# Kernel optimization log

Hardware: AMD Instinct MI355X
Metric: run time of the kernel (lower is better)

## Reference

```python
import jax, jax.numpy as jnp
import numpy as np
from jax import lax

# 4D convolution via lax.conv_general_dilated (supports N spatial dims natively)
# Layout: x is (N, C, T, U, V, W); weight is (O, I, kT, kU, kV, kW)

def conv4d(x, w, b):
    dn = lax.conv_dimension_numbers(x.shape, w.shape, ('NCTUVW', 'OITUVW', 'NCTUVW'))
    y = lax.conv_general_dilated(x, w, window_strides=(1, 1, 1, 1), padding='SAME',
                                 dimension_numbers=dn)
    return y + b[None, :, None, None, None, None]


def setup_inputs() -> dict:
    key = jax.random.key(0)
    k0, k1, k2, k3, k4 = jax.random.split(key, 5)
    B, C_in, C_hid, C_out = 2, 64, 128, 64
    T, D, H, W = 4, 16, 32, 32
    K = 3  # kernel size per dim (stmode 'C' -> (3,3,3,3))
    x = jax.random.normal(k0, (B, C_in, T, D, H, W), dtype=jnp.float32)
    scale1 = 1.0 / np.sqrt(C_in * K ** 4)
    scale2 = 1.0 / np.sqrt(C_hid * K ** 4)
    w1 = jax.random.normal(k1, (C_hid, C_in, K, K, K, K), dtype=jnp.float32) * scale1
    b1 = jax.random.normal(k2, (C_hid,), dtype=jnp.float32) * scale1
    w2 = jax.random.normal(k3, (C_out, C_hid, K, K, K, K), dtype=jnp.float32) * scale2
    b2 = jax.random.normal(k4, (C_out,), dtype=jnp.float32) * scale2
    return {"x": x, "w1": w1, "b1": b1, "w2": w2, "b2": b2}


def reference(x, w1, b1, w2, b2):
    # conv1 -> ReLU -> (dropout p=0 is identity) -> conv2 -> (dropout identity)
    h = jax.nn.relu(conv4d(x, w1, b1))
    return conv4d(h, w2, b2)
```

## Files before the change

### kernel.cpp

```cpp
#include <hip/hip_runtime.h>


using bf16x8 = __attribute__((ext_vector_type(8))) __bf16;
using f32x16 = __attribute__((ext_vector_type(16))) float;
using f32x4  = __attribute__((ext_vector_type(4))) float;

typedef __attribute__((address_space(1))) const void as1_void;
typedef __attribute__((address_space(3))) void as3_void;
__device__ __forceinline__ void gload_lds16(const void* g, void* l) {
    __builtin_amdgcn_global_load_lds((as1_void*)g, (as3_void*)l, 16, 0, 0);
}

__global__ __launch_bounds__(256) void cvt_x(const float* __restrict__ x,
                                             __bf16* __restrict__ x_t) {
    __shared__ float lt[64][65];
    const int nb = blockIdx.y;
    const int p0 = blockIdx.x * 64;
    const int tu = p0 >> 10;
    const float* src = x + (size_t)nb * 64 * 65536;
    __bf16* dst = x_t + (size_t)nb * 65536 * 64;
    #pragma unroll
    for (int i = 0; i < 16; ++i) {
        int idx = i * 256 + threadIdx.x;
        int c = idx >> 6, p = idx & 63;
        lt[c][p] = src[(size_t)c * 65536 + p0 + p];
    }
    __syncthreads();
    #pragma unroll
    for (int i = 0; i < 16; ++i) {
        int idx = i * 256 + threadIdx.x;
        int c = idx >> 6, pl = idx & 63;
        int p = p0 + pl;
        int v = (p >> 5) & 31, w = p & 31;
        dst[(size_t)(tu * 32 + v) * 2048 + (c >> 3) * 256 + w * 8 + (c & 7)] =
            (__bf16)lt[c][pl];
    }
}

template <int CIN>
__global__ __launch_bounds__(256) void cvt_w(const float* __restrict__ w,
                                             __bf16* __restrict__ wt) {
    constexpr int LOG = (CIN == 64) ? 6 : 7;
    constexpr int COUT = 8192 / CIN;
    int oc = blockIdx.x * 256 + threadIdx.x;
    if (oc >= 8192) return;
    const int o = oc >> LOG, c = oc & (CIN - 1);
    const int kg = c >> 4, cl = c & 15;
    const float* src = w + (size_t)oc * 81;
    #pragma unroll 1
    for (int tap = 0; tap < 81; ++tap)
        wt[(((size_t)tap * (CIN / 16) + kg) * COUT + o) * 16 + cl] = (__bf16)src[tap];
}

template <int CIN, int COUT, int NT, int WPEU, bool RELU>
__global__ __launch_bounds__(256, WPEU) void conv4d_mfma(
    const __bf16* __restrict__ in_t,
    const __bf16* __restrict__ wt,
    const float* __restrict__ bias,
    __bf16* __restrict__ out_bf,
    float* __restrict__ out_f)
{
    constexpr int KST   = CIN / 16;
    constexpr int UNITS = CIN / 32;
    constexpr int LOGU  = (UNITS == 2) ? 1 : 2;
    __shared__ __bf16 tile[2 * 6528];

    const int tid  = threadIdx.x;
    const int lane = tid & 63;
    const int l31  = lane & 31;
    const int hl   = lane >> 5;
    const int wv   = tid >> 6;
    const int gmi  = wv >> 1;
    const int gni  = wv & 1;

    const int bid = blockIdx.x;
    const int xcd = bid & 7;
    const int s0  = bid >> 3;
    const int u   = xcd * 2 + (s0 & 1);
    const int vg  = (s0 >> 1) & 7;
    const int t   = (s0 >> 4) & 3;
    const int nb  = (s0 >> 6) & 1;
    const int v0  = vg * 4;
    const int pbase = ((t * 16 + u) * 32 + v0) * 32;

    const __bf16* inb = in_t + (size_t)nb * 65536 * CIN;

    int goff[4];
    #pragma unroll
    for (int r = 0; r < 4; ++r) {
        const int slot = r * 256 + tid;
        const int row  = slot / 136;
        const int rem  = slot - row * 136;
        const int chunk = rem / 34;
        const int wp   = rem - chunk * 34;
        const int v_in = v0 - 1 + row;
        const int w_in = wp - 1;
        const bool ok = (row < 6) && ((unsigned)v_in < 32u) && ((unsigned)w_in < 32u);
        goff[r] = ok ? (v_in * (CIN * 32) + chunk * 256 + w_in * 8) : -1;
    }

    #pragma unroll
    for (int r = 0; r < 4; ++r) {
        const int slot = r * 256 + tid;
        if (slot < 816 && goff[r] < 0) {
            *(uint4*)((char*)tile + slot * 16) = make_uint4(0u, 0u, 0u, 0u);
            *(uint4*)((char*)tile + 13056 + slot * 16) = make_uint4(0u, 0u, 0u, 0u);
        }
    }

    const int lane_base = gmi * 2 * 136 + hl * 34 + l31;
    const bf16x8* tile16 = (const bf16x8*)tile;

    const __bf16* wlane[NT];
    #pragma unroll
    for (int nt = 0; nt < NT; ++nt)
        wlane[nt] = wt + ((gni * NT + nt) * 32 + l31) * 16 + hl * 8;

    int sb[9], tb0[9], nst = 0;
    #pragma unroll
    for (int kt = 0; kt < 3; ++kt) {
        const int t_in = t + kt - 1;
        if ((unsigned)t_in >= 4u) continue;
        #pragma unroll
        for (int ku = 0; ku < 3; ++ku) {
            const int u_in = u + ku - 1;
            if ((unsigned)u_in >= 16u) continue;
            sb[nst]  = (t_in * 16 + u_in) * 1024 * CIN;
            tb0[nst] = (kt * 3 + ku) * 9;
            ++nst;
        }
    }
    const int U = nst * UNITS;

    f32x16 acc[2][NT];
    #pragma unroll
    for (int mt = 0; mt < 2; ++mt)
        #pragma unroll
        for (int nt = 0; nt < NT; ++nt)
            #pragma unroll
            for (int i = 0; i < 16; ++i)
                acc[mt][nt][i] = 0.f;

    auto issue = [&](int j) {
        const int st = j >> LOGU, ch = j & (UNITS - 1);
        const __bf16* gb = inb + sb[st] + ch * 1024;
        char* lb = ((char*)tile) + (j & 1) * 13056 + wv * 1024;
        #pragma unroll
        for (int r = 0; r < 4; ++r)
            if (goff[r] >= 0)
                gload_lds16(gb + goff[r], lb + r * 4096);
    };

    issue(0);
    #pragma unroll 1
    for (int i = 0; i < U; ++i) {
        asm volatile("s_waitcnt vmcnt(0) lgkmcnt(0)" ::: "memory");
        __syncthreads();
        if (i + 1 < U) issue(i + 1);

        const int st = i >> LOGU, ch = i & (UNITS - 1);
        const int tapb = tb0[st];
        const bf16x8* tb = tile16 + (i & 1) * 816 + lane_base;
        #pragma unroll
        for (int ks = 0; ks < 2; ++ks) {
            const int ksg = ch * 2 + ks;
            #pragma unroll
            for (int kw = 0; kw < 3; ++kw) {
                bf16x8 af[4];
                #pragma unroll
                for (int r = 0; r < 4; ++r)
                    af[r] = tb[r * 136 + ks * 68 + kw];
                bf16x8 bv[3][NT];
                #pragma unroll
                for (int kv = 0; kv < 3; ++kv) {
                    const size_t wo =
                        ((size_t)(tapb + kv * 3 + kw) * KST + ksg) * (COUT * 16);
                    #pragma unroll
                    for (int nt = 0; nt < NT; ++nt)
                        bv[kv][nt] = *(const bf16x8*)(wlane[nt] + wo);
                }
                #pragma unroll
                for (int kv = 0; kv < 3; ++kv)
                    #pragma unroll
                    for (int rr = 0; rr < 2; ++rr)
                        #pragma unroll
                        for (int nt = 0; nt < NT; ++nt)
                            acc[rr][nt] = __builtin_amdgcn_mfma_f32_32x32x16_bf16(
                                af[rr + kv], bv[kv][nt], acc[rr][nt], 0, 0, 0);
            }
        }
    }

    #pragma unroll
    for (int nt = 0; nt < NT; ++nt) {
        const int o = (gni * NT + nt) * 32 + l31;
        const float bvls = bias[o];
        #pragma unroll
        for (int mt = 0; mt < 2; ++mt) {
            const int pb = pbase + (gmi * 2 + mt) * 32;
            if constexpr (RELU) {
                #pragma unroll
                for (int rg = 0; rg < 4; ++rg)
                    #pragma unroll
                    for (int j = 0; j < 4; ++j) {
                        float v = acc[mt][nt][rg * 4 + j] + bvls;
                        v = v > 0.f ? v : 0.f;
                        const int p = pb + j + 8 * rg + 4 * hl;
                        const int vv = (p >> 5) & 31, ww = p & 31, tu = p >> 10;
                        out_bf[(size_t)nb * 65536 * COUT +
                               (size_t)(tu * 32 + vv) * (32 * COUT) +
                               (o >> 3) * 256 + ww * 8 + (o & 7)] = (__bf16)v;
                    }
            } else {
                #pragma unroll
                for (int rg = 0; rg < 4; ++rg) {
                    f32x4 sv;
                    #pragma unroll
                    for (int j = 0; j < 4; ++j)
                        sv[j] = acc[mt][nt][rg * 4 + j] + bvls;
                    const int p = pb + 8 * rg + 4 * hl;
                    *(f32x4*)(out_f + ((size_t)nb * COUT + o) * 65536 + p) = sv;
                }
            }
        }
    }
}

extern "C" void kernel_launch(void* const* d_in, const int* in_sizes, int n_in,
                              void* d_out, int out_size, void* d_ws, size_t ws_size,
                              hipStream_t stream) {
    const float* x  = (const float*)d_in[0];
    const float* w1 = (const float*)d_in[1];
    const float* b1 = (const float*)d_in[2];
    const float* w2 = (const float*)d_in[3];
    const float* b2 = (const float*)d_in[4];
    float* out = (float*)d_out;

    char* ws = (char*)d_ws;
    __bf16* x_t = (__bf16*)ws;
    __bf16* h_t = (__bf16*)(ws + 16777216);
    __bf16* w1t = (__bf16*)(ws + 50331648);
    __bf16* w2t = (__bf16*)(ws + 51658752);

    cvt_x<<<dim3(1024, 2), 256, 0, stream>>>(x, x_t);
    cvt_w<64><<<32, 256, 0, stream>>>(w1, w1t);
    cvt_w<128><<<32, 256, 0, stream>>>(w2, w2t);

    conv4d_mfma<64, 128, 2, 3, true><<<1024, 256, 0, stream>>>(x_t, w1t, b1, h_t,
                                                               nullptr);
    conv4d_mfma<128, 64, 1, 4, false><<<1024, 256, 0, stream>>>(h_t, w2t, b2, nullptr,
                                                                out);
}
```

Baseline: 397.8 us.

## Drop LDS staging in conv kernels, load activations directly from global

The conv kernel no longer stages input slabs into double-buffered LDS with async global-to-LDS loads and barriers. Each lane now reads its A fragments straight from global memory, using bounds masks for padding. The second conv switches to a 4x1 wave layout with NT=2 and half as many blocks. The weight conversion kernel is reorganised to run one block per tap. This removes the barrier and LDS overhead but gives up data reuse through LDS, so cache traffic rises and load latency is exposed.

New measurement: 632.8 us. +59.1%, slower.

```diff
diff --git a/kernel.cpp b/kernel.cpp
--- a/kernel.cpp
+++ b/kernel.cpp
@@ -4,12 +4,6 @@
 using bf16x8 = __attribute__((ext_vector_type(8))) __bf16;
 using f32x16 = __attribute__((ext_vector_type(16))) float;
 using f32x4  = __attribute__((ext_vector_type(4))) float;
-
-typedef __attribute__((address_space(1))) const void as1_void;
-typedef __attribute__((address_space(3))) void as3_void;
-__device__ __forceinline__ void gload_lds16(const void* g, void* l) {
-    __builtin_amdgcn_global_load_lds((as1_void*)g, (as3_void*)l, 16, 0, 0);
-}
 
 __global__ __launch_bounds__(256) void cvt_x(const float* __restrict__ x,
                                              __bf16* __restrict__ x_t) {
@@ -40,20 +34,22 @@
 template <int CIN>
 __global__ __launch_bounds__(256) void cvt_w(const float* __restrict__ w,
                                              __bf16* __restrict__ wt) {
-    constexpr int LOG = (CIN == 64) ? 6 : 7;
     constexpr int COUT = 8192 / CIN;
-    int oc = blockIdx.x * 256 + threadIdx.x;
-    if (oc >= 8192) return;
-    const int o = oc >> LOG, c = oc & (CIN - 1);
-    const int kg = c >> 4, cl = c & 15;
-    const float* src = w + (size_t)oc * 81;
-    #pragma unroll 1
-    for (int tap = 0; tap < 81; ++tap)
-        wt[(((size_t)tap * (CIN / 16) + kg) * COUT + o) * 16 + cl] = (__bf16)src[tap];
-}
-
-template <int CIN, int COUT, int NT, int WPEU, bool RELU>
-__global__ __launch_bounds__(256, WPEU) void conv4d_mfma(
+    constexpr int LOGC = (CIN == 64) ? 7 : 6;
+    const int tap = blockIdx.x;
+    __bf16* dst = wt + (size_t)tap * 8192;
+    #pragma unroll
+    for (int it = 0; it < 32; ++it) {
+        const int i  = it * 256 + threadIdx.x;
+        const int cl = i & 15;
+        const int o  = (i >> 4) & (COUT - 1);
+        const int kg = i >> (4 + LOGC);
+        dst[i] = (__bf16)w[(size_t)(o * CIN + kg * 16 + cl) * 81 + tap];
+    }
+}
+
+template <int CIN, int COUT, int WM, int WN, int NT, bool RELU>
+__global__ __launch_bounds__(256, 3) void conv4d_mfma(
     const __bf16* __restrict__ in_t,
     const __bf16* __restrict__ wt,
     const float* __restrict__ bias,
@@ -61,55 +57,45 @@
     float* __restrict__ out_f)
 {
     constexpr int KST   = CIN / 16;
-    constexpr int UNITS = CIN / 32;
-    constexpr int LOGU  = (UNITS == 2) ? 1 : 2;
-    __shared__ __bf16 tile[2 * 6528];
+    constexpr int VSPAN = WM * 2;
+    constexpr int VGB   = (VSPAN == 4) ? 3 : 2;
 
     const int tid  = threadIdx.x;
     const int lane = tid & 63;
     const int l31  = lane & 31;
     const int hl   = lane >> 5;
     const int wv   = tid >> 6;
-    const int gmi  = wv >> 1;
-    const int gni  = wv & 1;
+    const int gmi  = (WN == 2) ? (wv >> 1) : wv;
+    const int gni  = (WN == 2) ? (wv & 1) : 0;
 
     const int bid = blockIdx.x;
     const int xcd = bid & 7;
     const int s0  = bid >> 3;
     const int u   = xcd * 2 + (s0 & 1);
-    const int vg  = (s0 >> 1) & 7;
-    const int t   = (s0 >> 4) & 3;
-    const int nb  = (s0 >> 6) & 1;
-    const int v0  = vg * 4;
+    const int vg  = (s0 >> 1) & ((1 << VGB) - 1);
+    const int t   = (s0 >> (1 + VGB)) & 3;
+    const int nb  = (s0 >> (3 + VGB)) & 1;
+    const int v0  = vg * VSPAN;
     const int pbase = ((t * 16 + u) * 32 + v0) * 32;
 
     const __bf16* inb = in_t + (size_t)nb * 65536 * CIN;
 
-    int goff[4];
+    int  wloff[3];
+    bool wok[3];
+    #pragma unroll
+    for (int kw = 0; kw < 3; ++kw) {
+        const int w_in = l31 + kw - 1;
+        wok[kw]   = (unsigned)w_in < 32u;
+        wloff[kw] = hl * 256 + w_in * 8;
+    }
+    int  voff[4];
+    bool vok[4];
     #pragma unroll
     for (int r = 0; r < 4; ++r) {
-        const int slot = r * 256 + tid;
-        const int row  = slot / 136;
-        const int rem  = slot - row * 136;
-        const int chunk = rem / 34;
-        const int wp   = rem - chunk * 34;
-        const int v_in = v0 - 1 + row;
-        const int w_in = wp - 1;
-        const bool ok = (row < 6) && ((unsigned)v_in < 32u) && ((unsigned)w_in < 32u);
-        goff[r] = ok ? (v_in * (CIN * 32) + chunk * 256 + w_in * 8) : -1;
-    }
-
-    #pragma unroll
-    for (int r = 0; r < 4; ++r) {
-        const int slot = r * 256 + tid;
-        if (slot < 816 && goff[r] < 0) {
-            *(uint4*)((char*)tile + slot * 16) = make_uint4(0u, 0u, 0u, 0u);
-            *(uint4*)((char*)tile + 13056 + slot * 16) = make_uint4(0u, 0u, 0u, 0u);
-        }
-    }
-
-    const int lane_base = gmi * 2 * 136 + hl * 34 + l31;
-    const bf16x8* tile16 = (const bf16x8*)tile;
+        const int v_in = v0 - 1 + gmi * 2 + r;
+        vok[r]  = (unsigned)v_in < 32u;
+        voff[r] = v_in * (CIN * 32);
+    }
 
     const __bf16* wlane[NT];
     #pragma unroll
@@ -130,7 +116,10 @@
             ++nst;
         }
     }
-    const int U = nst * UNITS;
+
+    bf16x8 zf;
+    #pragma unroll
+    for (int j = 0; j < 8; ++j) zf[j] = (__bf16)0.f;
 
     f32x16 acc[2][NT];
     #pragma unroll
@@ -141,40 +130,27 @@
             for (int i = 0; i < 16; ++i)
                 acc[mt][nt][i] = 0.f;
 
-    auto issue = [&](int j) {
-        const int st = j >> LOGU, ch = j & (UNITS - 1);
-        const __bf16* gb = inb + sb[st] + ch * 1024;
-        char* lb = ((char*)tile) + (j & 1) * 13056 + wv * 1024;
-        #pragma unroll
-        for (int r = 0; r < 4; ++r)
-            if (goff[r] >= 0)
-                gload_lds16(gb + goff[r], lb + r * 4096);
-    };
-
-    issue(0);
     #pragma unroll 1
-    for (int i = 0; i < U; ++i) {
-        asm volatile("s_waitcnt vmcnt(0) lgkmcnt(0)" ::: "memory");
-        __syncthreads();
-        if (i + 1 < U) issue(i + 1);
-
-        const int st = i >> LOGU, ch = i & (UNITS - 1);
+    for (int st = 0; st < nst; ++st) {
+        const __bf16* ibase = inb + sb[st];
         const int tapb = tb0[st];
-        const bf16x8* tb = tile16 + (i & 1) * 816 + lane_base;
-        #pragma unroll
-        for (int ks = 0; ks < 2; ++ks) {
-            const int ksg = ch * 2 + ks;
+        #pragma unroll 2
+        for (int ksg = 0; ksg < KST; ++ksg) {
+            const __bf16* kbase = ibase + ksg * 512;
             #pragma unroll
             for (int kw = 0; kw < 3; ++kw) {
                 bf16x8 af[4];
                 #pragma unroll
-                for (int r = 0; r < 4; ++r)
-                    af[r] = tb[r * 136 + ks * 68 + kw];
+                for (int r = 0; r < 4; ++r) {
+                    const bool ok = vok[r] && wok[kw];
+                    const int off = ok ? (voff[r] + wloff[kw]) : 0;
+                    bf16x8 v = *(const bf16x8*)(kbase + off);
+                    af[r] = ok ? v : zf;
+                }
                 bf16x8 bv[3][NT];
                 #pragma unroll
                 for (int kv = 0; kv < 3; ++kv) {
-                    const size_t wo =
-                        ((size_t)(tapb + kv * 3 + kw) * KST + ksg) * (COUT * 16);
+                    const int wo = ((tapb + kv * 3 + kw) * KST + ksg) * (COUT * 16);
                     #pragma unroll
                     for (int nt = 0; nt < NT; ++nt)
                         bv[kv][nt] = *(const bf16x8*)(wlane[nt] + wo);
@@ -243,11 +219,11 @@
     __bf16* w2t = (__bf16*)(ws + 51658752);
 
     cvt_x<<<dim3(1024, 2), 256, 0, stream>>>(x, x_t);
-    cvt_w<64><<<32, 256, 0, stream>>>(w1, w1t);
-    cvt_w<128><<<32, 256, 0, stream>>>(w2, w2t);
-
-    conv4d_mfma<64, 128, 2, 3, true><<<1024, 256, 0, stream>>>(x_t, w1t, b1, h_t,
-                                                               nullptr);
-    conv4d_mfma<128, 64, 1, 4, false><<<1024, 256, 0, stream>>>(h_t, w2t, b2, nullptr,
-                                                                out);
-}
+    cvt_w<64><<<81, 256, 0, stream>>>(w1, w1t);
+    cvt_w<128><<<81, 256, 0, stream>>>(w2, w2t);
+
+    conv4d_mfma<64, 128, 2, 2, 2, true><<<1024, 256, 0, stream>>>(x_t, w1t, b1, h_t,
+                                                                  nullptr);
+    conv4d_mfma<128, 64, 4, 1, 2, false><<<512, 256, 0, stream>>>(h_t, w2t, b2,
+                                                                  nullptr, out);
+}
```

## Give each wave a private LDS input tile and drop block barriers

Applied to the files above, without the earlier changes.

Each wave now stages only the input rows it consumes into its own double-buffered LDS region, so the per-iteration __syncthreads is replaced by a per-wave vmcnt wait. This removes block-wide synchronisation in the main loop, at the cost of duplicated global loads for the overlapping halo rows and larger LDS use, which caps occupancy at two blocks per CU. The weight conversion kernel is also reorganised to write one tap per block with coalesced stores, and the weight offset arithmetic moves to 32-bit.

Measured after the change: 479.1 us. 20.5% more time.

```diff
diff --git a/kernel.cpp b/kernel.cpp
--- a/kernel.cpp
+++ b/kernel.cpp
@@ -40,20 +40,22 @@
 template <int CIN>
 __global__ __launch_bounds__(256) void cvt_w(const float* __restrict__ w,
                                              __bf16* __restrict__ wt) {
-    constexpr int LOG = (CIN == 64) ? 6 : 7;
     constexpr int COUT = 8192 / CIN;
-    int oc = blockIdx.x * 256 + threadIdx.x;
-    if (oc >= 8192) return;
-    const int o = oc >> LOG, c = oc & (CIN - 1);
-    const int kg = c >> 4, cl = c & 15;
-    const float* src = w + (size_t)oc * 81;
-    #pragma unroll 1
-    for (int tap = 0; tap < 81; ++tap)
-        wt[(((size_t)tap * (CIN / 16) + kg) * COUT + o) * 16 + cl] = (__bf16)src[tap];
-}
-
-template <int CIN, int COUT, int NT, int WPEU, bool RELU>
-__global__ __launch_bounds__(256, WPEU) void conv4d_mfma(
+    constexpr int LOGC = (CIN == 64) ? 7 : 6;
+    const int tap = blockIdx.x;
+    __bf16* dst = wt + (size_t)tap * 8192;
+    #pragma unroll
+    for (int it = 0; it < 32; ++it) {
+        const int i  = it * 256 + threadIdx.x;
+        const int cl = i & 15;
+        const int o  = (i >> 4) & (COUT - 1);
+        const int kg = i >> (4 + LOGC);
+        dst[i] = (__bf16)w[(size_t)(o * CIN + kg * 16 + cl) * 81 + tap];
+    }
+}
+
+template <int CIN, int COUT, int NT, bool RELU>
+__global__ __launch_bounds__(256, 2) void conv4d_mfma(
     const __bf16* __restrict__ in_t,
     const __bf16* __restrict__ wt,
     const float* __restrict__ bias,
@@ -63,7 +65,7 @@
     constexpr int KST   = CIN / 16;
     constexpr int UNITS = CIN / 32;
     constexpr int LOGU  = (UNITS == 2) ? 1 : 2;
-    __shared__ __bf16 tile[2 * 6528];
+    __shared__ __bf16 tile[4 * 1088 * 8];
 
     const int tid  = threadIdx.x;
     const int lane = tid & 63;
@@ -85,31 +87,34 @@
 
     const __bf16* inb = in_t + (size_t)nb * 65536 * CIN;
 
-    int goff[4];
-    #pragma unroll
-    for (int r = 0; r < 4; ++r) {
-        const int slot = r * 256 + tid;
+    int goff[9];
+    #pragma unroll
+    for (int r = 0; r < 9; ++r) {
+        const int slot = r * 64 + lane;
         const int row  = slot / 136;
         const int rem  = slot - row * 136;
         const int chunk = rem / 34;
         const int wp   = rem - chunk * 34;
-        const int v_in = v0 - 1 + row;
+        const int v_in = v0 - 1 + gmi * 2 + row;
         const int w_in = wp - 1;
-        const bool ok = (row < 6) && ((unsigned)v_in < 32u) && ((unsigned)w_in < 32u);
+        const bool ok = (slot < 544) && ((unsigned)v_in < 32u) &&
+                        ((unsigned)w_in < 32u);
         goff[r] = ok ? (v_in * (CIN * 32) + chunk * 256 + w_in * 8) : -1;
     }
 
-    #pragma unroll
-    for (int r = 0; r < 4; ++r) {
-        const int slot = r * 256 + tid;
-        if (slot < 816 && goff[r] < 0) {
-            *(uint4*)((char*)tile + slot * 16) = make_uint4(0u, 0u, 0u, 0u);
-            *(uint4*)((char*)tile + 13056 + slot * 16) = make_uint4(0u, 0u, 0u, 0u);
-        }
-    }
-
-    const int lane_base = gmi * 2 * 136 + hl * 34 + l31;
-    const bf16x8* tile16 = (const bf16x8*)tile;
+    char* mybuf = (char*)tile + wv * 17408;
+    #pragma unroll
+    for (int r = 0; r < 9; ++r) {
+        const int slot = r * 64 + lane;
+        if (slot < 544 && goff[r] < 0) {
+            *(uint4*)(mybuf + slot * 16) = make_uint4(0u, 0u, 0u, 0u);
+            *(uint4*)(mybuf + 8704 + slot * 16) = make_uint4(0u, 0u, 0u, 0u);
+        }
+    }
+    asm volatile("s_waitcnt lgkmcnt(0)" ::: "memory");
+
+    const bf16x8* mybuf16 = (const bf16x8*)mybuf;
+    const int lane_base = hl * 34 + l31;
 
     const __bf16* wlane[NT];
     #pragma unroll
@@ -144,23 +149,22 @@
     auto issue = [&](int j) {
         const int st = j >> LOGU, ch = j & (UNITS - 1);
         const __bf16* gb = inb + sb[st] + ch * 1024;
-        char* lb = ((char*)tile) + (j & 1) * 13056 + wv * 1024;
-        #pragma unroll
-        for (int r = 0; r < 4; ++r)
+        char* lb = mybuf + (j & 1) * 8704;
+        #pragma unroll
+        for (int r = 0; r < 9; ++r)
             if (goff[r] >= 0)
-                gload_lds16(gb + goff[r], lb + r * 4096);
+                gload_lds16(gb + goff[r], lb + r * 1024);
     };
 
     issue(0);
     #pragma unroll 1
     for (int i = 0; i < U; ++i) {
-        asm volatile("s_waitcnt vmcnt(0) lgkmcnt(0)" ::: "memory");
-        __syncthreads();
+        asm volatile("s_waitcnt vmcnt(0)" ::: "memory");
         if (i + 1 < U) issue(i + 1);
 
         const int st = i >> LOGU, ch = i & (UNITS - 1);
         const int tapb = tb0[st];
-        const bf16x8* tb = tile16 + (i & 1) * 816 + lane_base;
+        const bf16x8* tb = mybuf16 + (i & 1) * 544 + lane_base;
         #pragma unroll
         for (int ks = 0; ks < 2; ++ks) {
             const int ksg = ch * 2 + ks;
@@ -173,8 +177,7 @@
                 bf16x8 bv[3][NT];
                 #pragma unroll
                 for (int kv = 0; kv < 3; ++kv) {
-                    const size_t wo =
-                        ((size_t)(tapb + kv * 3 + kw) * KST + ksg) * (COUT * 16);
+                    const int wo = ((tapb + kv * 3 + kw) * KST + ksg) * (COUT * 16);
                     #pragma unroll
                     for (int nt = 0; nt < NT; ++nt)
                         bv[kv][nt] = *(const bf16x8*)(wlane[nt] + wo);
@@ -243,11 +246,11 @@
     __bf16* w2t = (__bf16*)(ws + 51658752);
 
     cvt_x<<<dim3(1024, 2), 256, 0, stream>>>(x, x_t);
-    cvt_w<64><<<32, 256, 0, stream>>>(w1, w1t);
-    cvt_w<128><<<32, 256, 0, stream>>>(w2, w2t);
-
-    conv4d_mfma<64, 128, 2, 3, true><<<1024, 256, 0, stream>>>(x_t, w1t, b1, h_t,
-                                                               nullptr);
-    conv4d_mfma<128, 64, 1, 4, false><<<1024, 256, 0, stream>>>(h_t, w2t, b2, nullptr,
-                                                                out);
-}
+    cvt_w<64><<<81, 256, 0, stream>>>(w1, w1t);
+    cvt_w<128><<<81, 256, 0, stream>>>(w2, w2t);
+
+    conv4d_mfma<64, 128, 2, true><<<1024, 256, 0, stream>>>(x_t, w1t, b1, h_t,
+                                                            nullptr);
+    conv4d_mfma<128, 64, 1, false><<<1024, 256, 0, stream>>>(h_t, w2t, b2, nullptr,
+                                                             out);
+}
```
